# Kernel tuning notes

Hardware: AMD Instinct MI355X
Metric: run time of the kernel (lower is better)

The kernel has to match this reference:

```python
import jax, jax.numpy as jnp
import numpy as np

HEADS = 8
DIM_HEAD = 64
SCALE = DIM_HEAD ** -0.5

def setup_inputs() -> dict:
    key = jax.random.key(0)
    ks = jax.random.split(key, 6)
    b, n, m, qd, cd = 4, 2048, 2048, 256, 256
    inner = HEADS * DIM_HEAD
    return {
        "x": jax.random.normal(ks[0], (b, n, qd), jnp.float32),
        "context": jax.random.normal(ks[1], (b, m, cd), jnp.float32),
        "Wq": jax.random.normal(ks[2], (inner, qd), jnp.float32) * 0.02,
        "bq": jnp.zeros((inner,), jnp.float32),
        "Wkv": jax.random.normal(ks[3], (2 * inner, cd), jnp.float32) * 0.02,
        "bkv": jnp.zeros((2 * inner,), jnp.float32),
        "Wo": jax.random.normal(ks[4], (qd, inner), jnp.float32) * 0.02,
        "bo": jnp.zeros((qd,), jnp.float32),
    }

def reference(x, context, Wq, bq, Wkv, bkv, Wo, bo):
    b, n, _ = x.shape
    m = context.shape[1]
    inner = HEADS * DIM_HEAD
    # 1x1 conv projections == pointwise linear
    q = jnp.einsum('bnd,ed->bne', x, Wq) + bq            # [b, n, inner]
    kv = jnp.einsum('bmd,ed->bme', context, Wkv) + bkv    # [b, m, 2*inner]
    k, v = kv[..., :inner], kv[..., inner:]
    q = q.reshape(b, n, HEADS, DIM_HEAD).transpose(0, 2, 1, 3)  # [b,h,n,d]
    k = k.reshape(b, m, HEADS, DIM_HEAD).transpose(0, 2, 1, 3)
    v = v.reshape(b, m, HEADS, DIM_HEAD).transpose(0, 2, 1, 3)
    sim = jnp.einsum('bhid,bhjd->bhij', q, k) * SCALE     # [b,h,n,m]
    attn = jax.nn.softmax(sim, axis=-1)
    out = jnp.einsum('bhij,bhjd->bhid', attn, v)          # [b,h,n,d]
    out = out.transpose(0, 2, 1, 3).reshape(b, n, inner)  # [b,n,inner]
    return jnp.einsum('bne,oe->bno', out, Wo) + bo        # [b,n,query_dim]
```

## Files before the change

### kernel.cpp

```cpp
#include <hip/hip_runtime.h>
#include <hip/hip_bf16.h>

#define NB 4
#define SEQ 2048
#define NHEADS 8
#define ROWS (NB * SEQ)

typedef __attribute__((ext_vector_type(8))) short bf16x8;
typedef __attribute__((ext_vector_type(4))) short bf16x4;
typedef __attribute__((ext_vector_type(4))) float f32x4;
typedef __attribute__((ext_vector_type(16))) float f32x16;

__device__ inline short f2bf(float x) {
    union { float f; unsigned u; } v; v.f = x;
    unsigned r = v.u + 0x7FFF + ((v.u >> 16) & 1);
    return (short)(r >> 16);
}

__device__ inline unsigned pack2bf(float a, float b) {
    __hip_bfloat162 h = __float22bfloat162_rn(make_float2(a, b));
    unsigned u; __builtin_memcpy(&u, &h, 4);
    return u;
}

__device__ inline unsigned comb2(unsigned w1, unsigned w2, float inv) {
    union { unsigned v; float f; } a, b, c, d;
    a.v = w1 << 16;          b.v = w2 << 16;
    c.v = w1 & 0xffff0000u;  d.v = w2 & 0xffff0000u;
    return pack2bf((a.f + b.f) * inv, (c.f + d.f) * inv);
}

__global__ __launch_bounds__(256) void cvt_all(
    const float* __restrict__ x, const float* __restrict__ ctx,
    const float* __restrict__ wq, const float* __restrict__ wkv,
    const float* __restrict__ wo,
    short* __restrict__ xb, short* __restrict__ cb, short* __restrict__ wqb,
    short* __restrict__ wkvb, short* __restrict__ wob)
{
    const int i = blockIdx.x * 256 + threadIdx.x;
    const float* src; short* dst; int off;
    if (i < 524288)       { src = x;   dst = xb;   off = i; }
    else if (i < 1048576) { src = ctx; dst = cb;   off = i - 524288; }
    else if (i < 1081344) { src = wq;  dst = wqb;  off = i - 1048576; }
    else if (i < 1146880) { src = wkv; dst = wkvb; off = i - 1081344; }
    else                  { src = wo;  dst = wob;  off = i - 1146880; }
    const float4 v = ((const float4*)src)[off];
    uint2 o2;
    o2.x = pack2bf(v.x, v.y);
    o2.y = pack2bf(v.z, v.w);
    *(uint2*)(dst + (size_t)off * 4) = o2;
}

__global__ __launch_bounds__(256, 3) void proj2(
    const short* __restrict__ xb, const short* __restrict__ wqb,
    const float* __restrict__ bq,
    const short* __restrict__ cb, const short* __restrict__ wkvb,
    const float* __restrict__ bkv,
    short* __restrict__ q2b, short* __restrict__ kv2b, float qscale)
{
    __shared__ short As[128 * 64];
    __shared__ short Ws[128 * 64];
    const int tid = threadIdx.x;
    const int bid = blockIdx.x;
    const int w = tid >> 6, lane = tid & 63, low = lane & 15, quad = lane >> 4;
    const int wm = w >> 1, wn = w & 1;
    const int K = 256;

    const short* A; const short* W; const float* bias;
    short* outp; int Ccols; float scale; int rM0, c0;
    if (bid < 512) {
        A = cb; W = wkvb; bias = bkv; outp = kv2b; Ccols = 1024; scale = 1.0f;
        c0 = (bid & 7) * 128; rM0 = (bid >> 3) * 128;
    } else {
        const int u = bid - 512;
        A = xb; W = wqb; bias = bq; outp = q2b; Ccols = 512; scale = qscale;
        c0 = (u & 3) * 128; rM0 = (u >> 2) * 128;
    }

    const int srow = tid >> 3, sj = tid & 7;

    f32x4 acc[4][4];
#pragma unroll
    for (int mt = 0; mt < 4; ++mt)
#pragma unroll
        for (int nt = 0; nt < 4; ++nt) acc[mt][nt] = (f32x4){0.f, 0.f, 0.f, 0.f};

    bf16x8 pab[4], pwb[4];
#pragma unroll
    for (int c = 0; c < 4; ++c) {
        const int row = c * 32 + srow;
        pab[c] = *(const bf16x8*)(A + (size_t)(rM0 + row) * K + sj * 8);
        pwb[c] = *(const bf16x8*)(W + (size_t)(c0 + row) * K + sj * 8);
    }

    int k0 = 0;
    for (;;) {
        __syncthreads();
#pragma unroll
        for (int c = 0; c < 4; ++c) {
            const int row = c * 32 + srow;
            const int pc = sj ^ (row & 7);
            *(bf16x8*)(&As[row * 64 + pc * 8]) = pab[c];
            *(bf16x8*)(&Ws[row * 64 + pc * 8]) = pwb[c];
        }
        __syncthreads();
        const int kn = k0 + 64;
        if (kn < K) {
#pragma unroll
            for (int c = 0; c < 4; ++c) {
                const int row = c * 32 + srow;
                pab[c] = *(const bf16x8*)(A + (size_t)(rM0 + row) * K + kn + sj * 8);
                pwb[c] = *(const bf16x8*)(W + (size_t)(c0 + row) * K + kn + sj * 8);
            }
        }
#pragma unroll
        for (int kh = 0; kh < 2; ++kh) {
            bf16x8 af[4], bfv[4];
#pragma unroll
            for (int t = 0; t < 4; ++t) {
                const int ra = wm * 64 + t * 16 + low;
                af[t] = *(const bf16x8*)(&As[ra * 64 + ((kh * 4 + quad) ^ (ra & 7)) * 8]);
                const int rb = wn * 64 + t * 16 + low;
                bfv[t] = *(const bf16x8*)(&Ws[rb * 64 + ((kh * 4 + quad) ^ (rb & 7)) * 8]);
            }
#pragma unroll
            for (int mt = 0; mt < 4; ++mt)
#pragma unroll
                for (int nt = 0; nt < 4; ++nt)
                    acc[mt][nt] = __builtin_amdgcn_mfma_f32_16x16x32_bf16(af[mt], bfv[nt], acc[mt][nt], 0, 0, 0);
        }
        k0 = kn;
        if (k0 >= K) break;
    }

#pragma unroll
    for (int nt = 0; nt < 4; ++nt) {
        const int col = c0 + wn * 64 + nt * 16 + low;
        const float bv = bias[col];
#pragma unroll
        for (int mt = 0; mt < 4; ++mt) {
            const size_t rbase = (size_t)(rM0 + wm * 64 + mt * 16 + quad * 4);
#pragma unroll
            for (int r = 0; r < 4; ++r)
                outp[(rbase + r) * Ccols + col] = f2bf((acc[mt][nt][r] + bv) * scale);
        }
    }
}

__global__ __launch_bounds__(256) void gemm64_ocomb(
    const short* __restrict__ num, const float* __restrict__ lbuf,
    const short* __restrict__ W, const float* __restrict__ bias,
    float* __restrict__ out)
{
    const int K = 512, Ccols = 256;
    const size_t NHALF = (size_t)ROWS * 512;
    const int R8 = ROWS * 8;
    __shared__ short As[64 * 64];
    __shared__ short Ws[64 * 64];
    const int tid = threadIdx.x;
    const int w = tid >> 6, lane = tid & 63, low = lane & 15, quad = lane >> 4;
    const int wm = w >> 1, wn = w & 1;
    const int r0 = blockIdx.y * 64, c0 = blockIdx.x * 64;
    const int srow = tid >> 2;
    const int sc = (tid & 3) * 2;

    f32x4 acc[2][2];
#pragma unroll
    for (int mt = 0; mt < 2; ++mt)
#pragma unroll
        for (int nt = 0; nt < 2; ++nt) acc[mt][nt] = (f32x4){0.f, 0.f, 0.f, 0.f};

    uint4 pa1[2], pa2[2];
    float pinv;
    bf16x8 pwb[2];

    auto loadA = [&](int k0) {
        const int hh = k0 >> 6;
        const int row = r0 + srow;
        pinv = lbuf[row * 8 + hh] + lbuf[R8 + row * 8 + hh];
        const short* p1 = num + (size_t)row * 512 + k0 + sc * 8;
        pa1[0] = ((const uint4*)p1)[0];
        pa1[1] = ((const uint4*)p1)[1];
        const short* p2 = p1 + NHALF;
        pa2[0] = ((const uint4*)p2)[0];
        pa2[1] = ((const uint4*)p2)[1];
    };
    auto loadW = [&](int k0) {
        const short* p = W + (size_t)(c0 + srow) * K + k0 + sc * 8;
        pwb[0] = ((const bf16x8*)p)[0];
        pwb[1] = ((const bf16x8*)p)[1];
    };

    loadA(0); loadW(0);

    int k0 = 0;
    for (;;) {
        __syncthreads();
        {
            const float inv = 1.f / pinv;
#pragma unroll
            for (int c = 0; c < 2; ++c) {
                const int pc = (sc + c) ^ (srow & 7);
                union { unsigned u[4]; bf16x8 v; } r;
                r.u[0] = comb2(pa1[c].x, pa2[c].x, inv);
                r.u[1] = comb2(pa1[c].y, pa2[c].y, inv);
                r.u[2] = comb2(pa1[c].z, pa2[c].z, inv);
                r.u[3] = comb2(pa1[c].w, pa2[c].w, inv);
                *(bf16x8*)(&As[srow * 64 + pc * 8]) = r.v;
                *(bf16x8*)(&Ws[srow * 64 + pc * 8]) = pwb[c];
            }
        }
        __syncthreads();
        const int kn = k0 + 64;
        if (kn < K) { loadA(kn); loadW(kn); }
#pragma unroll
        for (int kh = 0; kh < 2; ++kh) {
            bf16x8 af[2], bfv[2];
#pragma unroll
            for (int t = 0; t < 2; ++t) {
                const int ra = wm * 32 + t * 16 + low;
                af[t] = *(const bf16x8*)(&As[ra * 64 + ((kh * 4 + quad) ^ (ra & 7)) * 8]);
                const int rb = wn * 32 + t * 16 + low;
                bfv[t] = *(const bf16x8*)(&Ws[rb * 64 + ((kh * 4 + quad) ^ (rb & 7)) * 8]);
            }
#pragma unroll
            for (int mt = 0; mt < 2; ++mt)
#pragma unroll
                for (int nt = 0; nt < 2; ++nt)
                    acc[mt][nt] = __builtin_amdgcn_mfma_f32_16x16x32_bf16(af[mt], bfv[nt], acc[mt][nt], 0, 0, 0);
        }
        k0 = kn;
        if (k0 >= K) break;
    }

#pragma unroll
    for (int nt = 0; nt < 2; ++nt) {
        const int col = c0 + wn * 32 + nt * 16 + low;
        const float bv = bias[col];
#pragma unroll
        for (int mt = 0; mt < 2; ++mt) {
            const size_t rbase = (size_t)(r0 + wm * 32 + mt * 16 + quad * 4);
#pragma unroll
            for (int r = 0; r < 4; ++r)
                out[(rbase + r) * Ccols + col] = acc[mt][nt][r] + bv;
        }
    }
}

#define KST 72
#define VST 72

__global__ __launch_bounds__(256, 4) void attn_mfma(
    const short* __restrict__ q2,
    const short* __restrict__ kv2,
    short* __restrict__ numb,
    float* __restrict__ lbuf)
{
    __shared__ short Ks[64 * KST];
    __shared__ short Vt[64 * VST];

    const int tid = threadIdx.x;
    const int w = tid >> 6;
    const int lane = tid & 63;
    const int l31 = lane & 31;
    const int h2 = lane >> 5;

    const int flat = blockIdx.x;
    const int h = flat & 7;
    const int rest = flat >> 3;
    const int half = rest & 1;
    const int rest2 = rest >> 1;
    const int qtile = rest2 & 15;
    const int b = rest2 >> 4;
    const int iq0 = qtile * 128;
    const int jt0 = half * 16;

    bf16x8 qr[4];
#pragma unroll
    for (int st = 0; st < 4; ++st)
        qr[st] = *(const bf16x8*)(q2 + (size_t)(b * SEQ + iq0 + w * 32 + l31) * 512
                                  + h * 64 + st * 16 + h2 * 8);

    const short* kbase = kv2 + (size_t)(b * SEQ) * 1024 + h * 64;
    const short* vbase = kbase + 512;

    float lsum = 0.f;
    f32x16 oacc[2];
#pragma unroll
    for (int dg = 0; dg < 2; ++dg)
#pragma unroll
        for (int r = 0; r < 16; ++r) oacc[dg][r] = 0.f;

    const int krow = tid >> 2;
    const int kc = (tid & 3) * 16;
    const int vk4 = (tid & 15) * 4;
    const int vd4 = (tid >> 4) * 4;

    bf16x8 pk0, pk1;
    bf16x4 pv0, pv1, pv2, pv3;
    {
        const short* ksrc = kbase + (size_t)(jt0 * 64 + krow) * 1024 + kc;
        pk0 = *(const bf16x8*)(ksrc);
        pk1 = *(const bf16x8*)(ksrc + 8);
        const short* vs = vbase + (size_t)(jt0 * 64 + vk4) * 1024 + vd4;
        pv0 = *(const bf16x4*)(vs);
        pv1 = *(const bf16x4*)(vs + 1024);
        pv2 = *(const bf16x4*)(vs + 2048);
        pv3 = *(const bf16x4*)(vs + 3072);
    }

    for (int jt = jt0; jt < jt0 + 16; ++jt) {
        __syncthreads();
        *(bf16x8*)(&Ks[krow * KST + kc]) = pk0;
        *(bf16x8*)(&Ks[krow * KST + kc + 8]) = pk1;
        {
            bf16x4 c0_, c1_, c2_, c3_;
            c0_[0] = pv0[0]; c0_[1] = pv1[0]; c0_[2] = pv2[0]; c0_[3] = pv3[0];
            c1_[0] = pv0[1]; c1_[1] = pv1[1]; c1_[2] = pv2[1]; c1_[3] = pv3[1];
            c2_[0] = pv0[2]; c2_[1] = pv1[2]; c2_[2] = pv2[2]; c2_[3] = pv3[2];
            c3_[0] = pv0[3]; c3_[1] = pv1[3]; c3_[2] = pv2[3]; c3_[3] = pv3[3];
            *(bf16x4*)(&Vt[(vd4 + 0) * VST + vk4]) = c0_;
            *(bf16x4*)(&Vt[(vd4 + 1) * VST + vk4]) = c1_;
            *(bf16x4*)(&Vt[(vd4 + 2) * VST + vk4]) = c2_;
            *(bf16x4*)(&Vt[(vd4 + 3) * VST + vk4]) = c3_;
        }
        __syncthreads();

        if (jt + 1 < jt0 + 16) {
            const short* ksrc = kbase + (size_t)((jt + 1) * 64 + krow) * 1024 + kc;
            pk0 = *(const bf16x8*)(ksrc);
            pk1 = *(const bf16x8*)(ksrc + 8);
            const short* vs = vbase + (size_t)((jt + 1) * 64 + vk4) * 1024 + vd4;
            pv0 = *(const bf16x4*)(vs);
            pv1 = *(const bf16x4*)(vs + 1024);
            pv2 = *(const bf16x4*)(vs + 2048);
            pv3 = *(const bf16x4*)(vs + 3072);
        }

        bf16x8 pfrag[4];
#pragma unroll
        for (int kg = 0; kg < 2; ++kg) {
            f32x16 s;
#pragma unroll
            for (int r = 0; r < 16; ++r) s[r] = 0.f;
#pragma unroll
            for (int st = 0; st < 4; ++st) {
                const bf16x8 kf = *(const bf16x8*)(&Ks[(kg * 32 + l31) * KST + st * 16 + h2 * 8]);
                s = __builtin_amdgcn_mfma_f32_32x32x16_bf16(kf, qr[st], s, 0, 0, 0);
            }
            unsigned wv[8];
#pragma unroll
            for (int g = 0; g < 4; ++g) {
                const float p0 = __builtin_amdgcn_exp2f(s[4 * g + 0]);
                const float p1 = __builtin_amdgcn_exp2f(s[4 * g + 1]);
                const float p2 = __builtin_amdgcn_exp2f(s[4 * g + 2]);
                const float p3 = __builtin_amdgcn_exp2f(s[4 * g + 3]);
                lsum += (p0 + p1) + (p2 + p3);
                wv[2 * g]     = pack2bf(p0, p1);
                wv[2 * g + 1] = pack2bf(p2, p3);
            }
#pragma unroll
            for (int q = 0; q < 2; ++q) {
                unsigned a0 = wv[4 * q + 0], b0 = wv[4 * q + 2];
                unsigned a1 = wv[4 * q + 1], b1 = wv[4 * q + 3];
                asm volatile("v_permlane32_swap_b32 %0, %1" : "+v"(a0), "+v"(b0));
                asm volatile("v_permlane32_swap_b32 %0, %1" : "+v"(a1), "+v"(b1));
                union { unsigned u[4]; bf16x8 v; } f;
                f.u[0] = a0; f.u[1] = a1; f.u[2] = b0; f.u[3] = b1;
                pfrag[kg * 2 + q] = f.v;
            }
        }

#pragma unroll
        for (int st = 0; st < 4; ++st) {
            const bf16x8 pf = pfrag[st];
#pragma unroll
            for (int dg = 0; dg < 2; ++dg) {
                const bf16x8 vf = *(const bf16x8*)(&Vt[(dg * 32 + l31) * VST + st * 16 + h2 * 8]);
                oacc[dg] = __builtin_amdgcn_mfma_f32_32x32x16_bf16(pf, vf, oacc[dg], 0, 0, 0);
            }
        }
    }

    lsum += __shfl_xor(lsum, 32);
    short* nb = numb + (size_t)half * ROWS * 512;
    float* lb = lbuf + (size_t)half * ROWS * 8;
    if (lane < 32)
        lb[(size_t)(b * SEQ + iq0 + w * 32 + l31) * 8 + h] = lsum;
#pragma unroll
    for (int dg = 0; dg < 2; ++dg)
#pragma unroll
        for (int r = 0; r < 16; ++r) {
            const int qrow = w * 32 + (r & 3) + 8 * (r >> 2) + 4 * h2;
            nb[(size_t)(b * SEQ + iq0 + qrow) * 512 + h * 64 + dg * 32 + l31] =
                f2bf(oacc[dg][r]);
        }
}

extern "C" void kernel_launch(void* const* d_in, const int* in_sizes, int n_in,
                              void* d_out, int out_size, void* d_ws, size_t ws_size,
                              hipStream_t stream) {
    const float* x   = (const float*)d_in[0];
    const float* ctx = (const float*)d_in[1];
    const float* Wq  = (const float*)d_in[2];
    const float* bq  = (const float*)d_in[3];
    const float* Wkv = (const float*)d_in[4];
    const float* bkv = (const float*)d_in[5];
    const float* Wo  = (const float*)d_in[6];
    const float* bo  = (const float*)d_in[7];
    float* out = (float*)d_out;

    short* xb   = (short*)d_ws;
    short* cb   = xb + (size_t)ROWS * 256;
    short* wqb  = cb + (size_t)ROWS * 256;
    short* wkvb = wqb + 131072;
    short* wob  = wkvb + 262144;
    short* q2b  = wob + 131072;
    short* kv2b = q2b + (size_t)ROWS * 512;
    short* numb = kv2b + (size_t)ROWS * 1024;
    float* lbuf = (float*)(numb + (size_t)2 * ROWS * 512);

    const float qscale = 0.125f * 1.44269504088896f;

    cvt_all<<<4608, 256, 0, stream>>>(x, ctx, Wq, Wkv, Wo,
                                      xb, cb, wqb, wkvb, wob);
    proj2<<<768, 256, 0, stream>>>(xb, wqb, bq, cb, wkvb, bkv,
                                   q2b, kv2b, qscale);
    attn_mfma<<<NB * NHEADS * (SEQ / 128) * 2, 256, 0, stream>>>(
        q2b, kv2b, numb, lbuf);
    gemm64_ocomb<<<dim3(256 / 64, ROWS / 64), 256, 0, stream>>>(
        numb, lbuf, wob, bo, out);
}
```

Before: 154.2 us.

## Load K fragments directly into registers and double-buffer V in LDS

Result: slower. 258.2 us (+67.5%).

```diff
diff --git a/kernel.cpp b/kernel.cpp
--- a/kernel.cpp
+++ b/kernel.cpp
@@ -247,7 +247,6 @@
     }
 }
 
-#define KST 72
 #define VST 72
 
 __global__ __launch_bounds__(256, 4) void attn_mfma(
@@ -256,8 +255,7 @@
     short* __restrict__ numb,
     float* __restrict__ lbuf)
 {
-    __shared__ short Ks[64 * KST];
-    __shared__ short Vt[64 * VST];
+    __shared__ short Vt[2][64 * VST];
 
     const int tid = threadIdx.x;
     const int w = tid >> 6;
@@ -291,51 +289,53 @@
 #pragma unroll
         for (int r = 0; r < 16; ++r) oacc[dg][r] = 0.f;
 
-    const int krow = tid >> 2;
-    const int kc = (tid & 3) * 16;
     const int vk4 = (tid & 15) * 4;
     const int vd4 = (tid >> 4) * 4;
 
-    bf16x8 pk0, pk1;
+    const short* kfb = kbase + (size_t)l31 * 1024 + h2 * 8;
+
+    bf16x8 kreg[8];
+#pragma unroll
+    for (int kg = 0; kg < 2; ++kg)
+#pragma unroll
+        for (int st = 0; st < 4; ++st)
+            kreg[kg * 4 + st] =
+                *(const bf16x8*)(kfb + (size_t)(jt0 * 64 + kg * 32) * 1024 + st * 16);
+
     bf16x4 pv0, pv1, pv2, pv3;
     {
-        const short* ksrc = kbase + (size_t)(jt0 * 64 + krow) * 1024 + kc;
-        pk0 = *(const bf16x8*)(ksrc);
-        pk1 = *(const bf16x8*)(ksrc + 8);
         const short* vs = vbase + (size_t)(jt0 * 64 + vk4) * 1024 + vd4;
         pv0 = *(const bf16x4*)(vs);
         pv1 = *(const bf16x4*)(vs + 1024);
         pv2 = *(const bf16x4*)(vs + 2048);
         pv3 = *(const bf16x4*)(vs + 3072);
     }
-
+    {
+        bf16x4 c0_, c1_, c2_, c3_;
+        c0_[0] = pv0[0]; c0_[1] = pv1[0]; c0_[2] = pv2[0]; c0_[3] = pv3[0];
+        c1_[0] = pv0[1]; c1_[1] = pv1[1]; c1_[2] = pv2[1]; c1_[3] = pv3[1];
+        c2_[0] = pv0[2]; c2_[1] = pv1[2]; c2_[2] = pv2[2]; c2_[3] = pv3[2];
+        c3_[0] = pv0[3]; c3_[1] = pv1[3]; c3_[2] = pv2[3]; c3_[3] = pv3[3];
+        short* Vn = &Vt[0][0];
+        *(bf16x4*)(&Vn[(vd4 + 0) * VST + vk4]) = c0_;
+        *(bf16x4*)(&Vn[(vd4 + 1) * VST + vk4]) = c1_;
+        *(bf16x4*)(&Vn[(vd4 + 2) * VST + vk4]) = c2_;
+        *(bf16x4*)(&Vn[(vd4 + 3) * VST + vk4]) = c3_;
+    }
+    __syncthreads();
+
+    int buf = 0;
     for (int jt = jt0; jt < jt0 + 16; ++jt) {
-        __syncthreads();
-        *(bf16x8*)(&Ks[krow * KST + kc]) = pk0;
-        *(bf16x8*)(&Ks[krow * KST + kc + 8]) = pk1;
-        {
-            bf16x4 c0_, c1_, c2_, c3_;
-            c0_[0] = pv0[0]; c0_[1] = pv1[0]; c0_[2] = pv2[0]; c0_[3] = pv3[0];
-            c1_[0] = pv0[1]; c1_[1] = pv1[1]; c1_[2] = pv2[1]; c1_[3] = pv3[1];
-            c2_[0] = pv0[2]; c2_[1] = pv1[2]; c2_[2] = pv2[2]; c2_[3] = pv3[2];
-            c3_[0] = pv0[3]; c3_[1] = pv1[3]; c3_[2] = pv2[3]; c3_[3] = pv3[3];
-            *(bf16x4*)(&Vt[(vd4 + 0) * VST + vk4]) = c0_;
-            *(bf16x4*)(&Vt[(vd4 + 1) * VST + vk4]) = c1_;
-            *(bf16x4*)(&Vt[(vd4 + 2) * VST + vk4]) = c2_;
-            *(bf16x4*)(&Vt[(vd4 + 3) * VST + vk4]) = c3_;
-        }
-        __syncthreads();
-
-        if (jt + 1 < jt0 + 16) {
-            const short* ksrc = kbase + (size_t)((jt + 1) * 64 + krow) * 1024 + kc;
-            pk0 = *(const bf16x8*)(ksrc);
-            pk1 = *(const bf16x8*)(ksrc + 8);
+        const bool notlast = (jt + 1 < jt0 + 16);
+
+        if (notlast) {
             const short* vs = vbase + (size_t)((jt + 1) * 64 + vk4) * 1024 + vd4;
             pv0 = *(const bf16x4*)(vs);
             pv1 = *(const bf16x4*)(vs + 1024);
             pv2 = *(const bf16x4*)(vs + 2048);
             pv3 = *(const bf16x4*)(vs + 3072);
         }
+        const short* kn = kfb + (size_t)((jt + 1) * 64) * 1024;
 
         bf16x8 pfrag[4];
 #pragma unroll
@@ -344,9 +344,13 @@
 #pragma unroll
             for (int r = 0; r < 16; ++r) s[r] = 0.f;
 #pragma unroll
-            for (int st = 0; st < 4; ++st) {
-                const bf16x8 kf = *(const bf16x8*)(&Ks[(kg * 32 + l31) * KST + st * 16 + h2 * 8]);
-                s = __builtin_amdgcn_mfma_f32_32x32x16_bf16(kf, qr[st], s, 0, 0, 0);
+            for (int st = 0; st < 4; ++st)
+                s = __builtin_amdgcn_mfma_f32_32x32x16_bf16(kreg[kg * 4 + st], qr[st], s, 0, 0, 0);
+            if (notlast) {
+#pragma unroll
+                for (int st = 0; st < 4; ++st)
+                    kreg[kg * 4 + st] =
+                        *(const bf16x8*)(kn + (size_t)(kg * 32) * 1024 + st * 16);
             }
             unsigned wv[8];
 #pragma unroll
@@ -371,15 +375,31 @@
             }
         }
 
+        const short* Vc = &Vt[buf][0];
 #pragma unroll
         for (int st = 0; st < 4; ++st) {
             const bf16x8 pf = pfrag[st];
 #pragma unroll
             for (int dg = 0; dg < 2; ++dg) {
-                const bf16x8 vf = *(const bf16x8*)(&Vt[(dg * 32 + l31) * VST + st * 16 + h2 * 8]);
+                const bf16x8 vf = *(const bf16x8*)(&Vc[(dg * 32 + l31) * VST + st * 16 + h2 * 8]);
                 oacc[dg] = __builtin_amdgcn_mfma_f32_32x32x16_bf16(pf, vf, oacc[dg], 0, 0, 0);
             }
         }
+
+        if (notlast) {
+            bf16x4 c0_, c1_, c2_, c3_;
+            c0_[0] = pv0[0]; c0_[1] = pv1[0]; c0_[2] = pv2[0]; c0_[3] = pv3[0];
+            c1_[0] = pv0[1]; c1_[1] = pv1[1]; c1_[2] = pv2[1]; c1_[3] = pv3[1];
+            c2_[0] = pv0[2]; c2_[1] = pv1[2]; c2_[2] = pv2[2]; c2_[3] = pv3[2];
+            c3_[0] = pv0[3]; c3_[1] = pv1[3]; c3_[2] = pv2[3]; c3_[3] = pv3[3];
+            short* Vn = &Vt[buf ^ 1][0];
+            *(bf16x4*)(&Vn[(vd4 + 0) * VST + vk4]) = c0_;
+            *(bf16x4*)(&Vn[(vd4 + 1) * VST + vk4]) = c1_;
+            *(bf16x4*)(&Vn[(vd4 + 2) * VST + vk4]) = c2_;
+            *(bf16x4*)(&Vn[(vd4 + 3) * VST + vk4]) = c3_;
+        }
+        __syncthreads();
+        buf ^= 1;
     }
 
     lsum += __shfl_xor(lsum, 32);
```

## Double-buffer LDS in output-projection GEMM and remap block order for locality

Applied to the files above, without the earlier changes.

Measured after the change: 152.5 us, median of 2. No clear change (-1.1%).

```diff
diff --git a/kernel.cpp b/kernel.cpp
--- a/kernel.cpp
+++ b/kernel.cpp
@@ -147,7 +147,7 @@
     }
 }
 
-__global__ __launch_bounds__(256) void gemm64_ocomb(
+__global__ __launch_bounds__(256, 2) void gemm64_ocomb(
     const short* __restrict__ num, const float* __restrict__ lbuf,
     const short* __restrict__ W, const float* __restrict__ bias,
     float* __restrict__ out)
@@ -155,12 +155,18 @@
     const int K = 512, Ccols = 256;
     const size_t NHALF = (size_t)ROWS * 512;
     const int R8 = ROWS * 8;
-    __shared__ short As[64 * 64];
-    __shared__ short Ws[64 * 64];
+    __shared__ short As[2][64 * 64];
+    __shared__ short Ws[2][64 * 64];
     const int tid = threadIdx.x;
     const int w = tid >> 6, lane = tid & 63, low = lane & 15, quad = lane >> 4;
     const int wm = w >> 1, wn = w & 1;
-    const int r0 = blockIdx.y * 64, c0 = blockIdx.x * 64;
+
+    const int d = blockIdx.x;
+    const int c8 = d & 7, j = d >> 3;
+    const int xcol = j & 3;
+    const int y = ((j >> 2) << 3) + c8;
+    const int r0 = y * 64, c0 = xcol * 64;
+
     const int srow = tid >> 2;
     const int sc = (tid & 3) * 2;
 
@@ -190,38 +196,40 @@
         pwb[0] = ((const bf16x8*)p)[0];
         pwb[1] = ((const bf16x8*)p)[1];
     };
+    auto stage = [&](int bi) {
+        const float inv = 1.f / pinv;
+#pragma unroll
+        for (int c = 0; c < 2; ++c) {
+            const int pc = (sc + c) ^ (srow & 7);
+            union { unsigned u[4]; bf16x8 v; } r;
+            r.u[0] = comb2(pa1[c].x, pa2[c].x, inv);
+            r.u[1] = comb2(pa1[c].y, pa2[c].y, inv);
+            r.u[2] = comb2(pa1[c].z, pa2[c].z, inv);
+            r.u[3] = comb2(pa1[c].w, pa2[c].w, inv);
+            *(bf16x8*)(&As[bi][srow * 64 + pc * 8]) = r.v;
+            *(bf16x8*)(&Ws[bi][srow * 64 + pc * 8]) = pwb[c];
+        }
+    };
 
     loadA(0); loadW(0);
-
-    int k0 = 0;
-    for (;;) {
-        __syncthreads();
-        {
-            const float inv = 1.f / pinv;
-#pragma unroll
-            for (int c = 0; c < 2; ++c) {
-                const int pc = (sc + c) ^ (srow & 7);
-                union { unsigned u[4]; bf16x8 v; } r;
-                r.u[0] = comb2(pa1[c].x, pa2[c].x, inv);
-                r.u[1] = comb2(pa1[c].y, pa2[c].y, inv);
-                r.u[2] = comb2(pa1[c].z, pa2[c].z, inv);
-                r.u[3] = comb2(pa1[c].w, pa2[c].w, inv);
-                *(bf16x8*)(&As[srow * 64 + pc * 8]) = r.v;
-                *(bf16x8*)(&Ws[srow * 64 + pc * 8]) = pwb[c];
-            }
-        }
-        __syncthreads();
-        const int kn = k0 + 64;
-        if (kn < K) { loadA(kn); loadW(kn); }
+    stage(0);
+    __syncthreads();
+
+    const int NT = K / 64;
+    for (int t = 0; t < NT; ++t) {
+        if (t + 1 < NT) { loadA((t + 1) * 64); loadW((t + 1) * 64); }
+
+        const short* Ac = &As[t & 1][0];
+        const short* Wc = &Ws[t & 1][0];
 #pragma unroll
         for (int kh = 0; kh < 2; ++kh) {
             bf16x8 af[2], bfv[2];
 #pragma unroll
-            for (int t = 0; t < 2; ++t) {
-                const int ra = wm * 32 + t * 16 + low;
-                af[t] = *(const bf16x8*)(&As[ra * 64 + ((kh * 4 + quad) ^ (ra & 7)) * 8]);
-                const int rb = wn * 32 + t * 16 + low;
-                bfv[t] = *(const bf16x8*)(&Ws[rb * 64 + ((kh * 4 + quad) ^ (rb & 7)) * 8]);
+            for (int tt = 0; tt < 2; ++tt) {
+                const int ra = wm * 32 + tt * 16 + low;
+                af[tt] = *(const bf16x8*)(&Ac[ra * 64 + ((kh * 4 + quad) ^ (ra & 7)) * 8]);
+                const int rb = wn * 32 + tt * 16 + low;
+                bfv[tt] = *(const bf16x8*)(&Wc[rb * 64 + ((kh * 4 + quad) ^ (rb & 7)) * 8]);
             }
 #pragma unroll
             for (int mt = 0; mt < 2; ++mt)
@@ -229,8 +237,9 @@
                 for (int nt = 0; nt < 2; ++nt)
                     acc[mt][nt] = __builtin_amdgcn_mfma_f32_16x16x32_bf16(af[mt], bfv[nt], acc[mt][nt], 0, 0, 0);
         }
-        k0 = kn;
-        if (k0 >= K) break;
+
+        if (t + 1 < NT) stage((t + 1) & 1);
+        __syncthreads();
     }
 
 #pragma unroll
@@ -428,6 +437,5 @@
                                    q2b, kv2b, qscale);
     attn_mfma<<<NB * NHEADS * (SEQ / 128) * 2, 256, 0, stream>>>(
         q2b, kv2b, numb, lbuf);
-    gemm64_ocomb<<<dim3(256 / 64, ROWS / 64), 256, 0, stream>>>(
-        numb, lbuf, wob, bo, out);
-}
+    gemm64_ocomb<<<512, 256, 0, stream>>>(numb, lbuf, wob, bo, out);
+}
```
